# Performance work log

Hardware: AMD Instinct MI355X
Metric: run time of the kernel (lower is better)

The kernel has to match this reference:

```python
import jax, jax.numpy as jnp
import numpy as np

B, T, H = 4, 512, 768
N, S = 256, 16
NER_DIM = 32
D = H + NER_DIM  # node_in_dim = 800
L, R = 2, 15
NE, MM = 64, 8
P = 1024
E = 4096
OUT = 97
NER_NUM = 7


def setup_inputs() -> dict:
    key = jax.random.key(0)
    ks = jax.random.split(key, 20)
    f = jax.random.normal
    inp = {}
    inp['token_feature'] = f(ks[0], (B, T, H), jnp.float32)
    inp['doc_cls_feature'] = f(ks[1], (B, H), jnp.float32)
    inp['node_span_pos'] = jax.random.randint(ks[2], (B, N, S), 0, T)
    inp['node_span_mask'] = jnp.ones((B, N, S), jnp.float32)
    inp['node_ner'] = jax.random.randint(ks[3], (B, N), 0, NER_NUM + 1)
    inp['node_mask'] = jnp.ones((B, N), jnp.float32)
    inp['ent2MentionId'] = jax.random.randint(ks[4], (B, NE, MM), 0, N + 1)
    inp['ent2MentionId_mask'] = jnp.ones((B, NE, MM), jnp.float32)
    inp['ent_pair'] = jax.random.randint(ks[5], (B, P, 2), 0, NE)
    inp['edge_src'] = jax.random.randint(ks[6], (B, E), 0, N)
    inp['edge_dst'] = jax.random.randint(ks[7], (B, E), 0, N)
    inp['edge_rel'] = jax.random.randint(ks[8], (B, E), 0, R)
    inp['ment_num'] = jax.random.randint(ks[9], (B,), 0, N)
    s = lambda k, sh: f(k, sh, jnp.float32) * 0.02
    inp['nerEmb'] = s(ks[10], (NER_NUM + 1, NER_DIM))
    inp['doc_W'] = s(ks[11], (H, D))
    inp['doc_b'] = jnp.zeros((D,), jnp.float32)
    inp['W_rel'] = s(ks[12], (L, R, D, D))
    inp['W_self'] = s(ks[13], (L, D, D))
    inp['gnn_b'] = jnp.zeros((L, D), jnp.float32)
    EE = 2 * D  # entity_embed_dim = 1600
    inp['W1'] = s(ks[14], (4 * EE, 2 * EE))
    inp['b1'] = jnp.zeros((2 * EE,), jnp.float32)
    inp['W2'] = s(ks[15], (2 * EE, OUT))
    inp['b2'] = jnp.zeros((OUT,), jnp.float32)
    return inp


def reference(token_feature, doc_cls_feature, node_span_pos, node_span_mask, node_ner,
              node_mask, ent2MentionId, ent2MentionId_mask, ent_pair, edge_src,
              edge_dst, edge_rel, ment_num, nerEmb, doc_W, doc_b, W_rel, W_self,
              gnn_b, W1, b1, W2, b2):
    # span pooling: gather span tokens, masked mean (avg pool with +0.1 denom as in source)
    span_tok = jax.vmap(lambda tf, p: tf[p])(token_feature, node_span_pos)  # [B,N,S,H]
    span = (span_tok * node_span_mask[..., None]).sum(2)
    span = span / (node_span_mask.sum(2, keepdims=True) + 0.1)
    node = span + doc_cls_feature[:, None, :]  # use_doc_feature add
    doc_proj = jax.nn.relu(doc_cls_feature @ doc_W + doc_b)  # doc_feature_fc
    node = jnp.concatenate([node, nerEmb[node_ner]], -1) * node_mask[..., None]  # [B,N,D]

    def per_sample(x, docp, m, src, dst, rel, e2m, e2m_mask, pairs):
        # node_in_feature[ment_num] = doc_cls_feature
        x = x.at[m].set(docp)
        outs = []
        h = x
        for l in range(L):
            # relational graph conv: per-relation transform then gather-scatter over edges
            Hr = jnp.einsum('nd,rde->rne', h, W_rel[l])  # [R,N,D]
            msg = Hr[rel, src]                            # [E,D]
            agg = jax.ops.segment_sum(msg, dst, num_segments=N)
            h = jax.nn.relu(agg + h @ W_self[l] + gnn_b[l])
            outs.append(h)
        on = jnp.concatenate([outs[0], outs[-1]], -1)     # [N,2D]
        on = jnp.concatenate([jnp.zeros((1, on.shape[-1]), on.dtype), on], 0)  # pad row 0
        ent = (on[e2m] * e2m_mask[..., None]).sum(1) / (e2m_mask.sum(1, keepdims=True) + 1e-7)
        hf = ent[pairs[:, 0]]
        tf_ = ent[pairs[:, 1]]
        feat = jnp.concatenate([hf, tf_, jnp.abs(hf - tf_), hf * tf_], -1)  # [P,4*EE]
        return jax.nn.relu(feat @ W1 + b1) @ W2 + b2       # [P,OUT]

    return jax.vmap(per_sample)(node, doc_proj, ment_num, edge_src, edge_dst,
                                edge_rel, ent2MentionId, ent2MentionId_mask, ent_pair)
```

## Files before the change

kernel.cpp:

```cpp
#include <hip/hip_runtime.h>
#include <hip/hip_bf16.h>

#define B_    4
#define T_    512
#define H_    768
#define N_    256
#define S_    16
#define NERD  32
#define D_    800
#define L_    2
#define R_    15
#define NE_   64
#define MM_   8
#define P_    1024
#define E_    4096
#define OUT_  97
#define NW    12800
#define EE2   1600
#define KF    (4 * EE2)
#define NH    (2 * EE2)
#define NPAD  3328
#define KS    800
#define NZ    4

typedef unsigned short u16;
typedef unsigned int   u32;
typedef __attribute__((ext_vector_type(8))) short  short8;
typedef __attribute__((ext_vector_type(4))) float  f32x4;

#define AS1 __attribute__((address_space(1)))
#define AS3 __attribute__((address_space(3)))

static __device__ __forceinline__ u16 f2bf(float f) {
  union { float f; u32 u; } v; v.f = f;
  u32 u = v.u;
  u32 r = (u + 0x7FFFu + ((u >> 16) & 1u)) >> 16;
  return (u16)r;
}
static __device__ __forceinline__ float bf2f(u16 h) {
  union { u32 u; float f; } v; v.u = ((u32)h) << 16;
  return v.f;
}

template <int OFS>
static __device__ __forceinline__ short8 dsr(u32 a) {
  short8 d;
  asm volatile("ds_read_b128 %0, %1 offset:%2" : "=v"(d) : "v"(a), "n"(OFS));
  return d;
}

__global__ __launch_bounds__(256) void k_doc_proj(
    const float* __restrict__ doc_cls, const float* __restrict__ doc_W,
    const float* __restrict__ doc_b, float* __restrict__ doc_proj) {
  int i = blockIdx.x * 256 + threadIdx.x;
  if (i >= B_ * D_) return;
  int b = i / D_, d = i % D_;
  float acc = doc_b[d];
  const float* dc = doc_cls + b * H_;
#pragma unroll 4
  for (int k = 0; k < H_; k++) acc += dc[k] * doc_W[k * D_ + d];
  doc_proj[i] = fmaxf(acc, 0.f);
}

__global__ __launch_bounds__(256) void k_build_node(
    const float* __restrict__ tokf, const float* __restrict__ doc_cls,
    const int* __restrict__ span_pos, const float* __restrict__ span_mask,
    const int* __restrict__ node_ner, const float* __restrict__ node_mask,
    const int* __restrict__ ment_num, const float* __restrict__ nerEmb,
    const float* __restrict__ doc_proj, u16* __restrict__ xB) {
  int n = blockIdx.x, b = blockIdx.y;
  __shared__ int pos_s[S_];
  __shared__ float msk_s[S_];
  int tid = threadIdx.x;
  if (tid < S_) {
    pos_s[tid] = span_pos[((size_t)b * N_ + n) * S_ + tid];
    msk_s[tid] = span_mask[((size_t)b * N_ + n) * S_ + tid];
  }
  __syncthreads();
  float msum = 0.f;
#pragma unroll
  for (int s = 0; s < S_; s++) msum += msk_s[s];
  float rinv = 1.f / (msum + 0.1f);
  int m = ment_num[b];
  float nm = node_mask[b * N_ + n];
  int ner = node_ner[b * N_ + n];
  for (int d = tid; d < D_; d += 256) {
    float v;
    if (d < H_) {
      float ssum = 0.f;
#pragma unroll
      for (int s = 0; s < S_; s++)
        ssum += tokf[((size_t)b * T_ + pos_s[s]) * H_ + d] * msk_s[s];
      v = ssum * rinv + doc_cls[b * H_ + d];
    } else {
      v = nerEmb[ner * NERD + (d - H_)];
    }
    v *= nm;
    if (n == m) v = doc_proj[b * D_ + d];
    xB[((size_t)b * N_ + n) * D_ + d] = f2bf(v);
  }
}

__global__ __launch_bounds__(256) void k_wt(const float* __restrict__ W_rel,
                                            const float* __restrict__ W_self,
                                            u16* __restrict__ WT) {
  __shared__ float tile[32][33];
  int l = blockIdx.z >> 4, i = blockIdx.z & 15;
  const float* src = (i < 15) ? (W_rel + ((size_t)l * R_ + i) * D_ * D_)
                              : (W_self + (size_t)l * D_ * D_);
  u16* dst = WT + (size_t)l * NW * D_ + (size_t)i * D_ * D_;
  int d0 = blockIdx.x * 32, e0 = blockIdx.y * 32;
  int tx = threadIdx.x & 31, ty = threadIdx.x >> 5;
  for (int j = ty; j < 32; j += 8)
    tile[j][tx] = src[(size_t)(d0 + j) * D_ + e0 + tx];
  __syncthreads();
  for (int j = ty; j < 32; j += 8)
    dst[(size_t)(e0 + j) * D_ + d0 + tx] = f2bf(tile[tx][j]);
}

__global__ __launch_bounds__(256) void k_w1t(const float* __restrict__ W1,
                                             u16* __restrict__ W1abT,
                                             u16* __restrict__ W1cdT) {
  __shared__ float tile[32][33];
  int k0 = blockIdx.x * 32, n0 = blockIdx.y * 32;
  int tx = threadIdx.x & 31, ty = threadIdx.x >> 5;
  for (int i = ty; i < 32; i += 8)
    tile[i][tx] = W1[(size_t)(k0 + i) * NH + n0 + tx];
  __syncthreads();
  for (int i = ty; i < 32; i += 8) {
    int kk = k0 + tx, n = n0 + i;
    u16 v = f2bf(tile[tx][i]);
    if (kk < EE2)            W1abT[(size_t)n * EE2 + kk] = v;
    else if (kk < 2 * EE2)   W1abT[(size_t)(NH + n) * EE2 + (kk - EE2)] = v;
    else                     W1cdT[(size_t)n * NH + (kk - 2 * EE2)] = v;
  }
}

__global__ __launch_bounds__(256) void k_w1cd_pad(u16* __restrict__ W1cdT) {
  size_t i = (size_t)blockIdx.x * 256 + threadIdx.x;
  ((u32*)(W1cdT + (size_t)NH * NH))[i] = 0u;
}

__global__ __launch_bounds__(256) void k_w2t(const float* __restrict__ W2,
                                             u16* __restrict__ W2T) {
  __shared__ float tile[32][33];
  int k0 = blockIdx.x * 32, n0 = blockIdx.y * 32;
  int tx = threadIdx.x & 31, ty = threadIdx.x >> 5;
  for (int i = ty; i < 32; i += 8)
    tile[i][tx] = (n0 + tx < OUT_) ? W2[(size_t)(k0 + i) * OUT_ + n0 + tx] : 0.f;
  __syncthreads();
  for (int i = ty; i < 32; i += 8)
    W2T[(size_t)(n0 + i) * NH + k0 + tx] = f2bf(tile[tx][i]);
}

__global__ __launch_bounds__(256) void k_csr_zero(int* __restrict__ cnt) {
  cnt[blockIdx.x * 256 + threadIdx.x] = 0;
}
__global__ __launch_bounds__(256) void k_csr_count(const int* __restrict__ edst,
                                                   int* __restrict__ cnt) {
  int e = blockIdx.x * 256 + threadIdx.x, b = blockIdx.y;
  atomicAdd(&cnt[b * N_ + edst[(size_t)b * E_ + e]], 1);
}
__global__ __launch_bounds__(256) void k_csr_scan(const int* __restrict__ cnt,
                                                  int* __restrict__ rowptr,
                                                  int* __restrict__ cursor) {
  int b = blockIdx.x, t = threadIdx.x;
  __shared__ int s[N_];
  int own = cnt[b * N_ + t];
  s[t] = own;
  __syncthreads();
  for (int off = 1; off < N_; off <<= 1) {
    int v = (t >= off) ? s[t - off] : 0;
    __syncthreads();
    s[t] += v;
    __syncthreads();
  }
  int excl = s[t] - own;
  rowptr[b * (N_ + 1) + t] = excl;
  cursor[b * N_ + t] = excl;
  if (t == 0) rowptr[b * (N_ + 1) + N_] = E_;
}
__global__ __launch_bounds__(256) void k_csr_fill(
    const int* __restrict__ esrc, const int* __restrict__ edst,
    const int* __restrict__ erel, int* __restrict__ cursor,
    int* __restrict__ elist) {
  int e = blockIdx.x * 256 + threadIdx.x, b = blockIdx.y;
  size_t ei = (size_t)b * E_ + e;
  int pos = atomicAdd(&cursor[b * N_ + edst[ei]], 1);
  elist[b * E_ + pos] = esrc[ei] | (erel[ei] << 9);
}

template <int KD, int EPI>
__global__ __launch_bounds__(256) void k_gemm_bt(
    const u16* __restrict__ A, int lda, const u16* __restrict__ Bm, int ldb,
    const float* __restrict__ bias, const float* __restrict__ preA,
    const float* __restrict__ preB, const int* __restrict__ pairs,
    void* __restrict__ Cv, int ldc, int ldpre, long long zA, long long zC) {
  __shared__ u16 As[128 * 32];
  __shared__ u16 Bs[128 * 32];
  int tid = threadIdx.x;
  int w = tid >> 6, lane = tid & 63;
  int wr = w >> 1, wc = w & 1;
  int lane16 = lane & 15, quad = lane >> 4;

  int nbn = gridDim.x, nbm = gridDim.y;
  int pid = blockIdx.y * nbn + blockIdx.x;
  const int GROUP = 8;
  int npg = GROUP * nbn;
  int gidg = pid / npg;
  int first = gidg * GROUP;
  int szm = min(nbm - first, GROUP);
  int pid_m = first + (pid % npg) % szm;
  int pid_n = (pid % npg) / szm;
  int n0 = pid_n * 128;
  int m0 = pid_m * 128;

  int lrow = lane >> 2;
  int lcol = (lane & 3) * 8;

  f32x4 acc[4][4] = {};

  const u16* gA = A + (size_t)blockIdx.z * zA + (size_t)m0 * lda;
  const u16* gB = Bm + (size_t)blockIdx.z * zA + (size_t)n0 * ldb;

  for (int kt = 0; kt < KD; kt += 32) {
    __syncthreads();
#pragma unroll
    for (int j = 0; j < 2; j++) {
      int chunk = j * 4 + w;
      int row = chunk * 16 + lrow;
      __builtin_amdgcn_global_load_lds(
          (const AS1 void*)(gA + (size_t)row * lda + kt + lcol),
          (AS3 void*)(As + chunk * 512 + lane * 8), 16, 0, 0);
      __builtin_amdgcn_global_load_lds(
          (const AS1 void*)(gB + (size_t)row * ldb + kt + lcol),
          (AS3 void*)(Bs + chunk * 512 + lane * 8), 16, 0, 0);
    }
    __syncthreads();

    short8 af[4], bf[4];
#pragma unroll
    for (int mi = 0; mi < 4; mi++) {
      int ml = wr * 64 + mi * 16 + lane16;
      af[mi] = *(const short8*)(As + ml * 32 + quad * 8);
    }
#pragma unroll
    for (int ni = 0; ni < 4; ni++) {
      int nl = wc * 64 + ni * 16 + lane16;
      bf[ni] = *(const short8*)(Bs + nl * 32 + quad * 8);
    }
#pragma unroll
    for (int mi = 0; mi < 4; mi++)
#pragma unroll
      for (int ni = 0; ni < 4; ni++)
        acc[mi][ni] = __builtin_amdgcn_mfma_f32_16x16x32_bf16(
            af[mi], bf[ni], acc[mi][ni], 0, 0, 0);
  }

  int cols[4];
  float bv[4];
#pragma unroll
  for (int ni = 0; ni < 4; ni++) {
    cols[ni] = n0 + wc * 64 + ni * 16 + lane16;
    if (EPI == 4) bv[ni] = (cols[ni] < NH) ? bias[cols[ni]] : 0.f;
  }
  float* Cf = (float*)Cv + (size_t)blockIdx.z * zC;
#pragma unroll
  for (int mi = 0; mi < 4; mi++) {
#pragma unroll
    for (int r = 0; r < 4; r++) {
      int row = m0 + wr * 64 + mi * 16 + quad * 4 + r;
#pragma unroll
      for (int ni = 0; ni < 4; ni++) {
        float v = acc[mi][ni][r];
        int col = cols[ni];
        if (EPI == 0) {
          ((u16*)Cv)[(size_t)row * ldc + col] = f2bf(v);
        } else if (EPI == 1) {
          Cf[(size_t)row * ldc + col] = v;
        } else if (EPI == 4) {
          Cf[(size_t)row * ldc + col] = v + bv[ni];
        }
      }
    }
  }
}

__global__ __launch_bounds__(512, 2) void k_gemm8p(
    const u16* __restrict__ A, const u16* __restrict__ Bm,
    const float* __restrict__ preAB_, const int* __restrict__ pairs,
    u16* __restrict__ C) {
  __shared__ u16 lds[2][2][2][128 * 64];

  int tid = threadIdx.x;
  int w = tid >> 6, lane = tid & 63;
  int wr = w >> 2, wc = w & 3;
  int lane16 = lane & 15, quad = lane >> 4;

  int pid = blockIdx.y * 13 + blockIdx.x;
  pid = (pid & 7) * 26 + (pid >> 3);
  int pid_m = pid / 13, pid_n = pid % 13;
  int m0 = pid_m * 256, n0 = pid_n * 256;

  int srow = (w << 3) + (lane >> 3);
  int g8 = ((lane & 7) ^ (lane >> 3)) << 3;
  const u16* gAt = A + (size_t)(m0 + srow) * NH + g8;
  const u16* gBt = Bm + (size_t)(n0 + srow) * NH + g8;
  int ldsSlot = ((w << 6) + lane) << 3;

#define STAGE(buf, ab, h, kt)                                                  \
  do {                                                                         \
    const u16* gsrc_ = (ab) ? gBt : gAt;                                       \
    __builtin_amdgcn_global_load_lds(                                          \
        (const AS1 void*)(gsrc_ + (size_t)((h)*128) * NH + (kt)),              \
        (AS3 void*)(&lds[buf][ab][h][0] + ldsSlot), 16, 0, 0);                 \
    __builtin_amdgcn_global_load_lds(                                          \
        (const AS1 void*)(gsrc_ + (size_t)((h)*128 + 64) * NH + (kt)),         \
        (AS3 void*)(&lds[buf][ab][h][0] + 4096 + ldsSlot), 16, 0, 0);          \
  } while (0)

  u32 ldsb = (u32)(size_t)&lds[0][0][0][0];
  u32 gk0 = (u32)((quad ^ (lane16 & 7)) << 4);
  u32 gk1 = (u32)(((4 + quad) ^ (lane16 & 7)) << 4);
  u32 aBase = ldsb + (u32)(wr * 16384) + (u32)(lane16 << 7);
  u32 bBase = ldsb + 32768u + (u32)((wc >> 1) * 16384) + (u32)((((wc & 1) << 6) + lane16) << 7);
  u32 aA0k0 = aBase + gk0,           aA0k1 = aBase + gk1;
  u32 aA1k0 = aA0k0 + 65536u,        aA1k1 = aA0k1 + 65536u;
  u32 bB0k0 = bBase + gk0,           bB0k1 = bBase + gk1;
  u32 bB1k0 = bB0k0 + 65536u,        bB1k1 = bB0k1 + 65536u;

#define RDA_ALL(A0, A1)                                      \
  a_[0][0] = dsr<0>(A0);     a_[0][1] = dsr<0>(A1);          \
  a_[1][0] = dsr<2048>(A0);  a_[1][1] = dsr<2048>(A1);       \
  a_[2][0] = dsr<4096>(A0);  a_[2][1] = dsr<4096>(A1);       \
  a_[3][0] = dsr<6144>(A0);  a_[3][1] = dsr<6144>(A1);       \
  a_[4][0] = dsr<8192>(A0);  a_[4][1] = dsr<8192>(A1);       \
  a_[5][0] = dsr<10240>(A0); a_[5][1] = dsr<10240>(A1);      \
  a_[6][0] = dsr<12288>(A0); a_[6][1] = dsr<12288>(A1);      \
  a_[7][0] = dsr<14336>(A0); a_[7][1] = dsr<14336>(A1);
#define RDB4(dst, Badr)                                      \
  dst[0] = dsr<0>(Badr);    dst[1] = dsr<2048>(Badr);        \
  dst[2] = dsr<4096>(Badr); dst[3] = dsr<6144>(Badr);

  f32x4 acc[8][4] = {};
  short8 a_[8][2];
  short8 b0_[4];
  short8 b1_[4];

  STAGE(0, 0, 0, 0); STAGE(0, 0, 1, 0); STAGE(0, 1, 0, 0); STAGE(0, 1, 1, 0);
  STAGE(1, 0, 0, 64); STAGE(1, 0, 1, 64); STAGE(1, 1, 0, 64);
  asm volatile("s_waitcnt vmcnt(6)");
  __builtin_amdgcn_s_barrier();

  const int NIT = NH / 128;
  for (int it = 0; it < NIT; ++it) {
    const int kbase = it * 128;
    const int kB1 = kbase + 64;
    const int kp2 = (it < NIT - 1) ? kbase + 128 : 0;
    const int kp3 = (it < NIT - 1) ? kbase + 192 : 0;
#pragma unroll
    for (int hv = 0; hv < 2; ++hv) {
      if (hv == 0) { RDA_ALL(aA0k0, aA0k1); RDB4(b0_, bB0k0); }
      else         { RDA_ALL(aA1k0, aA1k1); RDB4(b0_, bB1k0); }
      if (hv == 0) { STAGE(1, 1, 1, kB1); } else { STAGE(0, 1, 1, kp2); }
      __builtin_amdgcn_s_barrier();
      asm volatile("s_waitcnt lgkmcnt(0)");
      __builtin_amdgcn_sched_barrier(0);
      __builtin_amdgcn_s_setprio(1);
#pragma unroll
      for (int mi = 0; mi < 8; ++mi) {
        acc[mi][0] = __builtin_amdgcn_mfma_f32_16x16x32_bf16(a_[mi][0], b0_[0], acc[mi][0], 0, 0, 0);
        acc[mi][1] = __builtin_amdgcn_mfma_f32_16x16x32_bf16(a_[mi][0], b0_[1], acc[mi][1], 0, 0, 0);
      }
      __builtin_amdgcn_s_setprio(0);
      __builtin_amdgcn_s_barrier();

      if (hv == 0) { RDB4(b1_, bB0k1); } else { RDB4(b1_, bB1k1); }
      if (hv == 0) { STAGE(0, 0, 0, kp2); } else { STAGE(1, 0, 0, kp3); }
      __builtin_amdgcn_s_barrier();
      asm volatile("s_waitcnt lgkmcnt(0)");
      __builtin_amdgcn_sched_barrier(0);
      __builtin_amdgcn_s_setprio(1);
#pragma unroll
      for (int mi = 0; mi < 8; ++mi) {
        acc[mi][2] = __builtin_amdgcn_mfma_f32_16x16x32_bf16(a_[mi][0], b0_[2], acc[mi][2], 0, 0, 0);
        acc[mi][3] = __builtin_amdgcn_mfma_f32_16x16x32_bf16(a_[mi][0], b0_[3], acc[mi][3], 0, 0, 0);
      }
      __builtin_amdgcn_s_setprio(0);
      __builtin_amdgcn_s_barrier();

      if (hv == 0) { STAGE(0, 0, 1, kp2); } else { STAGE(1, 0, 1, kp3); }
      __builtin_amdgcn_s_barrier();
      __builtin_amdgcn_sched_barrier(0);
      __builtin_amdgcn_s_setprio(1);
#pragma unroll
      for (int mi = 0; mi < 8; ++mi) {
        acc[mi][0] = __builtin_amdgcn_mfma_f32_16x16x32_bf16(a_[mi][1], b1_[0], acc[mi][0], 0, 0, 0);
        acc[mi][1] = __builtin_amdgcn_mfma_f32_16x16x32_bf16(a_[mi][1], b1_[1], acc[mi][1], 0, 0, 0);
      }
      __builtin_amdgcn_s_setprio(0);
      __builtin_amdgcn_s_barrier();

      if (hv == 0) { STAGE(0, 1, 0, kp2); } else { STAGE(1, 1, 0, kp3); }
      __builtin_amdgcn_s_barrier();
      __builtin_amdgcn_sched_barrier(0);
      __builtin_amdgcn_s_setprio(1);
#pragma unroll
      for (int mi = 0; mi < 8; ++mi) {
        acc[mi][2] = __builtin_amdgcn_mfma_f32_16x16x32_bf16(a_[mi][1], b1_[2], acc[mi][2], 0, 0, 0);
        acc[mi][3] = __builtin_amdgcn_mfma_f32_16x16x32_bf16(a_[mi][1], b1_[3], acc[mi][3], 0, 0, 0);
      }
      __builtin_amdgcn_s_setprio(0);
      asm volatile("s_waitcnt vmcnt(6)");
      __builtin_amdgcn_s_barrier();
    }
  }
#undef STAGE
#undef RDA_ALL
#undef RDB4

#pragma unroll
  for (int mi = 0; mi < 8; ++mi) {
#pragma unroll
    for (int r = 0; r < 4; ++r) {
      int row = m0 + wr * 128 + mi * 16 + quad * 4 + r;
      int hp = pairs[2 * row], tp = pairs[2 * row + 1];
      int pb = (row >> 10) * NE_;
      const float* pAr = preAB_ + (size_t)(pb + hp) * KF;
      const float* pBr = preAB_ + NH + (size_t)(pb + tp) * KF;
#pragma unroll
      for (int ni = 0; ni < 4; ++ni) {
        int col = n0 + wc * 64 + ni * 16 + lane16;
        if (col < NH) {
          float v = acc[mi][ni][r] + pAr[col] + pBr[col];
          C[(size_t)row * NH + col] = f2bf(fmaxf(v, 0.f));
        }
      }
    }
  }
}

__global__ __launch_bounds__(128) void k_out_reduce(
    const float* __restrict__ part, const float* __restrict__ b2,
    float* __restrict__ out) {
  int row = blockIdx.x, c = threadIdx.x;
  if (c >= OUT_) return;
  float s = b2[c];
#pragma unroll
  for (int z = 0; z < NZ; z++)
    s += part[(size_t)z * (B_ * P_ * 128) + (size_t)row * 128 + c];
  out[(size_t)row * OUT_ + c] = s;
}

__global__ __launch_bounds__(256) void k_agg(
    const u16* __restrict__ Hr, const int* __restrict__ rowptr,
    const int* __restrict__ elist, const float* __restrict__ gnn_b, int layer,
    float* __restrict__ hout, u16* __restrict__ houtB) {
  int n = blockIdx.x, b = blockIdx.y;
  int beg = rowptr[b * (N_ + 1) + n], end = rowptr[b * (N_ + 1) + n + 1];
  const int* el = elist + (size_t)b * E_;
  const u16* HrB = Hr + (size_t)b * N_ * NW;
  int tid = threadIdx.x;
  for (int c = tid; c < D_; c += 256) {
    float acc = bf2f(HrB[(size_t)n * NW + R_ * D_ + c]) + gnn_b[layer * D_ + c];
    for (int i = beg; i < end; i++) {
      int pk = el[i];
      acc += bf2f(HrB[(size_t)(pk & 511) * NW + (pk >> 9) * D_ + c]);
    }
    float r = fmaxf(acc, 0.f);
    hout[((size_t)b * N_ + n) * D_ + c] = r;
    houtB[((size_t)b * N_ + n) * D_ + c] = f2bf(r);
  }
}

__global__ __launch_bounds__(256) void k_ent(
    const float* __restrict__ h0, const float* __restrict__ h1,
    const int* __restrict__ e2m, const float* __restrict__ e2m_mask,
    float* __restrict__ ent, u16* __restrict__ entB) {
  int e = blockIdx.x, b = blockIdx.y;
  __shared__ int idx_s[MM_];
  __shared__ float msk_s[MM_];
  int tid = threadIdx.x;
  if (tid < MM_) {
    idx_s[tid] = e2m[((size_t)b * NE_ + e) * MM_ + tid];
    msk_s[tid] = e2m_mask[((size_t)b * NE_ + e) * MM_ + tid];
  }
  __syncthreads();
  float msum = 0.f;
#pragma unroll
  for (int m = 0; m < MM_; m++) msum += msk_s[m];
  float inv = 1.f / (msum + 1e-7f);
  for (int c = tid; c < EE2; c += 256) {
    const float* base = (c < D_) ? h0 : h1;
    int cc = (c < D_) ? c : c - D_;
    float s = 0.f;
#pragma unroll
    for (int m = 0; m < MM_; m++) {
      int j = idx_s[m];
      if (j > 0) s += base[((size_t)b * N_ + (j - 1)) * D_ + cc] * msk_s[m];
    }
    float v = s * inv;
    ent[((size_t)b * NE_ + e) * EE2 + c] = v;
    entB[((size_t)b * NE_ + e) * EE2 + c] = f2bf(v);
  }
}

__global__ __launch_bounds__(256) void k_featC(
    const float* __restrict__ ent, const int* __restrict__ ent_pair,
    u16* __restrict__ featC) {
  int row = blockIdx.x;
  int b = row >> 10, g = row & 1023;
  int hp = ent_pair[(((size_t)b << 10) + g) * 2 + 0];
  int tp = ent_pair[(((size_t)b << 10) + g) * 2 + 1];
  const float* eh = ent + ((size_t)b * NE_ + hp) * EE2;
  const float* et = ent + ((size_t)b * NE_ + tp) * EE2;
  u16* orow = featC + (size_t)row * NH;
  for (int c = threadIdx.x; c < 800; c += 256) {
    int seg = c / 400, kk = (c - seg * 400) * 4;
    float4 hf = *(const float4*)(eh + kk);
    float4 tf = *(const float4*)(et + kk);
    float4 v;
    if (seg == 0) {
      v.x = fabsf(hf.x - tf.x); v.y = fabsf(hf.y - tf.y);
      v.z = fabsf(hf.z - tf.z); v.w = fabsf(hf.w - tf.w);
    } else {
      v.x = hf.x * tf.x; v.y = hf.y * tf.y;
      v.z = hf.z * tf.z; v.w = hf.w * tf.w;
    }
    ushort4 o;
    o.x = f2bf(v.x); o.y = f2bf(v.y); o.z = f2bf(v.z); o.w = f2bf(v.w);
    *(ushort4*)(orow + seg * EE2 + kk) = o;
  }
}

extern "C" void kernel_launch(void* const* d_in, const int* in_sizes, int n_in,
                              void* d_out, int out_size, void* d_ws, size_t ws_size,
                              hipStream_t stream) {
  const float* token_feature = (const float*)d_in[0];
  const float* doc_cls       = (const float*)d_in[1];
  const int*   span_pos      = (const int*)d_in[2];
  const float* span_mask     = (const float*)d_in[3];
  const int*   node_ner      = (const int*)d_in[4];
  const float* node_mask     = (const float*)d_in[5];
  const int*   e2m           = (const int*)d_in[6];
  const float* e2m_mask      = (const float*)d_in[7];
  const int*   ent_pair      = (const int*)d_in[8];
  const int*   edge_src      = (const int*)d_in[9];
  const int*   edge_dst      = (const int*)d_in[10];
  const int*   edge_rel      = (const int*)d_in[11];
  const int*   ment_num      = (const int*)d_in[12];
  const float* nerEmb        = (const float*)d_in[13];
  const float* doc_W         = (const float*)d_in[14];
  const float* doc_b         = (const float*)d_in[15];
  const float* W_rel         = (const float*)d_in[16];
  const float* W_self        = (const float*)d_in[17];
  const float* gnn_b         = (const float*)d_in[18];
  const float* W1            = (const float*)d_in[19];
  const float* b1            = (const float*)d_in[20];
  const float* W2            = (const float*)d_in[21];
  const float* b2            = (const float*)d_in[22];
  float* out = (float*)d_out;

  float* ws = (float*)d_ws;
  size_t off = 0;
  auto alloc = [&](size_t n) {
    float* p = ws + off;
    off += (n + 63) & ~size_t(63);
    return p;
  };
  float* doc_proj = alloc(B_ * D_);
  u16*   xB  = (u16*)alloc((size_t)B_ * N_ * D_ / 2);
  float* h0  = alloc((size_t)B_ * N_ * D_);
  float* h1  = alloc((size_t)B_ * N_ * D_);
  u16*   hB  = (u16*)alloc((size_t)B_ * N_ * D_ / 2);
  float* ent = alloc((size_t)B_ * NE_ * EE2);
  u16*   entB = (u16*)alloc((size_t)B_ * NE_ * EE2 / 2);
  u16*   WT    = (u16*)alloc((size_t)L_ * NW * D_ / 2);
  u16*   W1abT = (u16*)alloc((size_t)KF * EE2 / 2);
  u16*   W1cdT = (u16*)alloc((size_t)NPAD * NH / 2);
  u16*   W2T   = (u16*)alloc((size_t)128 * NH / 2);
  float* preAB = alloc((size_t)B_ * NE_ * KF);
  u16*   Hr    = (u16*)alloc((size_t)B_ * N_ * NW / 2);
  u16*   featC = Hr;
  u16*   hiddenB = (u16*)alloc((size_t)B_ * P_ * NH / 2);
  float* part    = alloc((size_t)NZ * B_ * P_ * 128);
  int*   csr_cnt    = (int*)alloc(B_ * N_ / 1 * sizeof(int) / 4);
  int*   csr_rowptr = (int*)alloc(B_ * (N_ + 1));
  int*   csr_cursor = (int*)alloc(B_ * N_);
  int*   csr_elist  = (int*)alloc(B_ * E_);
  (void)ws_size;

  k_csr_zero<<<dim3(B_), 256, 0, stream>>>(csr_cnt);
  k_csr_count<<<dim3(E_ / 256, B_), 256, 0, stream>>>(edge_dst, csr_cnt);
  k_csr_scan<<<dim3(B_), 256, 0, stream>>>(csr_cnt, csr_rowptr, csr_cursor);
  k_csr_fill<<<dim3(E_ / 256, B_), 256, 0, stream>>>(edge_src, edge_dst, edge_rel,
                                                     csr_cursor, csr_elist);

  k_wt<<<dim3(D_ / 32, D_ / 32, L_ * 16), 256, 0, stream>>>(W_rel, W_self, WT);
  k_w1t<<<dim3(KF / 32, NH / 32), 256, 0, stream>>>(W1, W1abT, W1cdT);
  k_w1cd_pad<<<dim3(800), 256, 0, stream>>>(W1cdT);
  k_w2t<<<dim3(NH / 32, 4), 256, 0, stream>>>(W2, W2T);

  k_doc_proj<<<dim3((B_ * D_ + 255) / 256), 256, 0, stream>>>(doc_cls, doc_W, doc_b, doc_proj);
  k_build_node<<<dim3(N_, B_), 256, 0, stream>>>(token_feature, doc_cls, span_pos, span_mask,
                                                 node_ner, node_mask, ment_num, nerEmb,
                                                 doc_proj, xB);
  const u16* hin = xB;
  float* houts[2] = {h0, h1};
  for (int l = 0; l < L_; l++) {
    k_gemm_bt<D_, 0><<<dim3(NW / 128, (B_ * N_) / 128), 256, 0, stream>>>(
        hin, D_, WT + (size_t)l * NW * D_, D_, nullptr, nullptr, nullptr, nullptr,
        Hr, NW, 0, 0, 0);
    k_agg<<<dim3(N_, B_), 256, 0, stream>>>(Hr, csr_rowptr, csr_elist,
                                            gnn_b, l, houts[l], hB);
    hin = hB;
  }
  k_ent<<<dim3(NE_, B_), 256, 0, stream>>>(h0, h1, e2m, e2m_mask, ent, entB);

  k_gemm_bt<EE2, 4><<<dim3(KF / 128, (B_ * NE_) / 128), 256, 0, stream>>>(
      entB, EE2, W1abT, EE2, b1, nullptr, nullptr, nullptr, preAB, KF, 0, 0, 0);

  k_featC<<<dim3(B_ * P_), 256, 0, stream>>>(ent, ent_pair, featC);

  k_gemm8p<<<dim3(NPAD / 256, (B_ * P_) / 256), 512, 0, stream>>>(
      featC, W1cdT, preAB, ent_pair, hiddenB);

  k_gemm_bt<KS, 1><<<dim3(1, (B_ * P_) / 128, NZ), 256, 0, stream>>>(
      hiddenB, NH, W2T, NH, nullptr, nullptr, nullptr, nullptr, part, 128,
      0, KS, (long long)B_ * P_ * 128);
  k_out_reduce<<<dim3(B_ * P_), 128, 0, stream>>>(part, b2, out);
}
```

Measured before the change: 795.0 us.

## Restructure GEMM K-tile into quadrant MFMA phases with reduced operand registers

```diff
diff --git a/kernel.cpp b/kernel.cpp
--- a/kernel.cpp
+++ b/kernel.cpp
@@ -329,95 +329,90 @@
   u32 bB0k0 = bBase + gk0,           bB0k1 = bBase + gk1;
   u32 bB1k0 = bB0k0 + 65536u,        bB1k1 = bB0k1 + 65536u;
 
-#define RDA_ALL(A0, A1)                                      \
-  a_[0][0] = dsr<0>(A0);     a_[0][1] = dsr<0>(A1);          \
-  a_[1][0] = dsr<2048>(A0);  a_[1][1] = dsr<2048>(A1);       \
-  a_[2][0] = dsr<4096>(A0);  a_[2][1] = dsr<4096>(A1);       \
-  a_[3][0] = dsr<6144>(A0);  a_[3][1] = dsr<6144>(A1);       \
-  a_[4][0] = dsr<8192>(A0);  a_[4][1] = dsr<8192>(A1);       \
-  a_[5][0] = dsr<10240>(A0); a_[5][1] = dsr<10240>(A1);      \
-  a_[6][0] = dsr<12288>(A0); a_[6][1] = dsr<12288>(A1);      \
-  a_[7][0] = dsr<14336>(A0); a_[7][1] = dsr<14336>(A1);
-#define RDB4(dst, Badr)                                      \
-  dst[0] = dsr<0>(Badr);    dst[1] = dsr<2048>(Badr);        \
-  dst[2] = dsr<4096>(Badr); dst[3] = dsr<6144>(Badr);
-
   f32x4 acc[8][4] = {};
-  short8 a_[8][2];
-  short8 b0_[4];
-  short8 b1_[4];
+  short8 a_[4][2];
+  short8 bL[2][2];
+  short8 bH[2][2];
+
+#define MMQ(MI0, NI0, BB)                                                      \
+  { _Pragma("unroll") for (int mi_ = 0; mi_ < 4; ++mi_) {                      \
+      _Pragma("unroll") for (int ni_ = 0; ni_ < 2; ++ni_) {                    \
+        f32x4 t_ = __builtin_amdgcn_mfma_f32_16x16x32_bf16(                    \
+            a_[mi_][0], BB[ni_][0], acc[(MI0) + mi_][(NI0) + ni_], 0, 0, 0);   \
+        acc[(MI0) + mi_][(NI0) + ni_] =                                        \
+            __builtin_amdgcn_mfma_f32_16x16x32_bf16(a_[mi_][1], BB[ni_][1],    \
+                                                    t_, 0, 0, 0);              \
+      } } }
+
+#define K_TILE(HB, OB, AK0, AK1, BK0, BK1, ktB1, kt2)                          \
+                           \
+  a_[0][0] = dsr<0>(AK0);    a_[0][1] = dsr<0>(AK1);                           \
+  a_[1][0] = dsr<2048>(AK0); a_[1][1] = dsr<2048>(AK1);                        \
+  a_[2][0] = dsr<4096>(AK0); a_[2][1] = dsr<4096>(AK1);                        \
+  a_[3][0] = dsr<6144>(AK0); a_[3][1] = dsr<6144>(AK1);                        \
+  bL[0][0] = dsr<0>(BK0);    bL[0][1] = dsr<0>(BK1);                           \
+  bL[1][0] = dsr<2048>(BK0); bL[1][1] = dsr<2048>(BK1);                        \
+  STAGE(OB, 1, 1, ktB1);                                                       \
+  asm volatile("s_waitcnt lgkmcnt(8)");                                        \
+  __builtin_amdgcn_s_barrier();                                                \
+  asm volatile("s_waitcnt lgkmcnt(0)");                                        \
+  __builtin_amdgcn_sched_barrier(0);                                           \
+  __builtin_amdgcn_s_setprio(1);                                               \
+  MMQ(0, 0, bL)                                                                \
+  __builtin_amdgcn_s_setprio(0);                                               \
+  __builtin_amdgcn_s_barrier();                                                \
+                                                         \
+  bH[0][0] = dsr<4096>(BK0); bH[0][1] = dsr<4096>(BK1);                        \
+  bH[1][0] = dsr<6144>(BK0); bH[1][1] = dsr<6144>(BK1);                        \
+  __builtin_amdgcn_s_barrier();                                                \
+  asm volatile("s_waitcnt lgkmcnt(0)");                                        \
+  __builtin_amdgcn_sched_barrier(0);                                           \
+  __builtin_amdgcn_s_setprio(1);                                               \
+  MMQ(0, 2, bH)                                                                \
+  __builtin_amdgcn_s_setprio(0);                                               \
+  __builtin_amdgcn_s_barrier();                                                \
+                 \
+  a_[0][0] = dsr<8192>(AK0);  a_[0][1] = dsr<8192>(AK1);                       \
+  a_[1][0] = dsr<10240>(AK0); a_[1][1] = dsr<10240>(AK1);                      \
+  a_[2][0] = dsr<12288>(AK0); a_[2][1] = dsr<12288>(AK1);                      \
+  a_[3][0] = dsr<14336>(AK0); a_[3][1] = dsr<14336>(AK1);                      \
+  STAGE(HB, 1, 0, kt2);                                                        \
+  __builtin_amdgcn_s_barrier();                                                \
+  asm volatile("s_waitcnt lgkmcnt(0)");                                        \
+  __builtin_amdgcn_sched_barrier(0);                                           \
+  __builtin_amdgcn_s_setprio(1);                                               \
+  MMQ(4, 2, bH)                                                                \
+  __builtin_amdgcn_s_setprio(0);                                               \
+  __builtin_amdgcn_s_barrier();                                                \
+           \
+  STAGE(HB, 0, 0, kt2);                                                        \
+  STAGE(HB, 0, 1, kt2);                                                        \
+  __builtin_amdgcn_s_barrier();                                                \
+  __builtin_amdgcn_sched_barrier(0);                                           \
+  __builtin_amdgcn_s_setprio(1);                                               \
+  MMQ(4, 0, bL)                                                                \
+  __builtin_amdgcn_s_setprio(0);                                               \
+  asm volatile("s_waitcnt vmcnt(6)");                                          \
+  __builtin_amdgcn_s_barrier();
 
   STAGE(0, 0, 0, 0); STAGE(0, 0, 1, 0); STAGE(0, 1, 0, 0); STAGE(0, 1, 1, 0);
-  STAGE(1, 0, 0, 64); STAGE(1, 0, 1, 64); STAGE(1, 1, 0, 64);
+  STAGE(1, 1, 0, 64); STAGE(1, 0, 0, 64); STAGE(1, 0, 1, 64);
   asm volatile("s_waitcnt vmcnt(6)");
   __builtin_amdgcn_s_barrier();
 
   const int NIT = NH / 128;
   for (int it = 0; it < NIT; ++it) {
     const int kbase = it * 128;
-    const int kB1 = kbase + 64;
-    const int kp2 = (it < NIT - 1) ? kbase + 128 : 0;
-    const int kp3 = (it < NIT - 1) ? kbase + 192 : 0;
-#pragma unroll
-    for (int hv = 0; hv < 2; ++hv) {
-      if (hv == 0) { RDA_ALL(aA0k0, aA0k1); RDB4(b0_, bB0k0); }
-      else         { RDA_ALL(aA1k0, aA1k1); RDB4(b0_, bB1k0); }
-      if (hv == 0) { STAGE(1, 1, 1, kB1); } else { STAGE(0, 1, 1, kp2); }
-      __builtin_amdgcn_s_barrier();
-      asm volatile("s_waitcnt lgkmcnt(0)");
-      __builtin_amdgcn_sched_barrier(0);
-      __builtin_amdgcn_s_setprio(1);
-#pragma unroll
-      for (int mi = 0; mi < 8; ++mi) {
-        acc[mi][0] = __builtin_amdgcn_mfma_f32_16x16x32_bf16(a_[mi][0], b0_[0], acc[mi][0], 0, 0, 0);
-        acc[mi][1] = __builtin_amdgcn_mfma_f32_16x16x32_bf16(a_[mi][0], b0_[1], acc[mi][1], 0, 0, 0);
-      }
-      __builtin_amdgcn_s_setprio(0);
-      __builtin_amdgcn_s_barrier();
-
-      if (hv == 0) { RDB4(b1_, bB0k1); } else { RDB4(b1_, bB1k1); }
-      if (hv == 0) { STAGE(0, 0, 0, kp2); } else { STAGE(1, 0, 0, kp3); }
-      __builtin_amdgcn_s_barrier();
-      asm volatile("s_waitcnt lgkmcnt(0)");
-      __builtin_amdgcn_sched_barrier(0);
-      __builtin_amdgcn_s_setprio(1);
-#pragma unroll
-      for (int mi = 0; mi < 8; ++mi) {
-        acc[mi][2] = __builtin_amdgcn_mfma_f32_16x16x32_bf16(a_[mi][0], b0_[2], acc[mi][2], 0, 0, 0);
-        acc[mi][3] = __builtin_amdgcn_mfma_f32_16x16x32_bf16(a_[mi][0], b0_[3], acc[mi][3], 0, 0, 0);
-      }
-      __builtin_amdgcn_s_setprio(0);
-      __builtin_amdgcn_s_barrier();
-
-      if (hv == 0) { STAGE(0, 0, 1, kp2); } else { STAGE(1, 0, 1, kp3); }
-      __builtin_amdgcn_s_barrier();
-      __builtin_amdgcn_sched_barrier(0);
-      __builtin_amdgcn_s_setprio(1);
-#pragma unroll
-      for (int mi = 0; mi < 8; ++mi) {
-        acc[mi][0] = __builtin_amdgcn_mfma_f32_16x16x32_bf16(a_[mi][1], b1_[0], acc[mi][0], 0, 0, 0);
-        acc[mi][1] = __builtin_amdgcn_mfma_f32_16x16x32_bf16(a_[mi][1], b1_[1], acc[mi][1], 0, 0, 0);
-      }
-      __builtin_amdgcn_s_setprio(0);
-      __builtin_amdgcn_s_barrier();
-
-      if (hv == 0) { STAGE(0, 1, 0, kp2); } else { STAGE(1, 1, 0, kp3); }
-      __builtin_amdgcn_s_barrier();
-      __builtin_amdgcn_sched_barrier(0);
-      __builtin_amdgcn_s_setprio(1);
-#pragma unroll
-      for (int mi = 0; mi < 8; ++mi) {
-        acc[mi][2] = __builtin_amdgcn_mfma_f32_16x16x32_bf16(a_[mi][1], b1_[2], acc[mi][2], 0, 0, 0);
-        acc[mi][3] = __builtin_amdgcn_mfma_f32_16x16x32_bf16(a_[mi][1], b1_[3], acc[mi][3], 0, 0, 0);
-      }
-      __builtin_amdgcn_s_setprio(0);
-      asm volatile("s_waitcnt vmcnt(6)");
-      __builtin_amdgcn_s_barrier();
-    }
+    const int kB1a = kbase + 64;
+    const int kt2a = (it < NIT - 1) ? kbase + 128 : 0;
+    const int kB1b = kt2a;
+    const int kt2b = (it < NIT - 1) ? kbase + 192 : 0;
+    K_TILE(0, 1, aA0k0, aA0k1, bB0k0, bB0k1, kB1a, kt2a)
+    K_TILE(1, 0, aA1k0, aA1k1, bB1k0, bB1k1, kB1b, kt2b)
   }
 #undef STAGE
-#undef RDA_ALL
-#undef RDB4
+#undef MMQ
+#undef K_TILE
 
 #pragma unroll
   for (int mi = 0; mi < 8; ++mi) {
```

Result: faster. 749.3 us (-5.8%).
